# Optimization experiments

Hardware: AMD Instinct MI355X
Metric: run time of the kernel (lower is better)

Reference implementation:

```python
import jax, jax.numpy as jnp
import numpy as np

TEMPERATURE = 0.07

def _l2norm(x):
    return x / jnp.linalg.norm(x, axis=-1, keepdims=True)

def setup_inputs() -> dict:
    key = jax.random.key(0)
    k1, k2, k3, k4 = jax.random.split(key, 4)
    B, T, C_ctx, C_enc, P, K = 8, 256, 512, 256, 12, 128
    context = jax.random.normal(k1, (B, T, C_ctx), dtype=jnp.float32)
    encoded = jax.random.normal(k2, (B, T, C_enc), dtype=jnp.float32)
    W = jax.random.normal(k3, (P, C_enc, C_ctx), dtype=jnp.float32) * (1.0 / np.sqrt(C_ctx))
    neg_idx = jax.random.randint(k4, (P, B * (T - 1), K), 0, B * T, dtype=jnp.int64)
    return {"context": context, "encoded": encoded, "W": W, "neg_idx": neg_idx}

def reference(context, encoded, W, neg_idx):
    B, T, C_enc = encoded.shape
    n_pred = W.shape[0]
    # normalized pool of all encoded vectors [B*T, C_enc]
    pool = _l2norm(encoded.reshape(B * T, C_enc))
    total = jnp.float32(0.0)
    for k in range(1, n_pred + 1):  # fixed small loop over horizons
        Nk = B * (T - k)
        c_t = context[:, : T - k, :]                       # [B, T-k, C_ctx]
        z_hat = jnp.einsum('btc,ec->bte', c_t, W[k - 1])   # [B, T-k, C_enc]
        z_hat = _l2norm(z_hat.reshape(Nk, C_enc))
        z_pos = _l2norm(encoded[:, k:, :].reshape(Nk, C_enc))
        pos_logits = jnp.sum(z_hat * z_pos, axis=-1, keepdims=True)  # [Nk, 1]
        z_neg = pool[neg_idx[k - 1, :Nk]]                  # [Nk, K, C_enc]
        neg_logits = jnp.einsum('nc,nkc->nk', z_hat, z_neg)
        logits = jnp.concatenate([pos_logits, neg_logits], axis=1) / TEMPERATURE
        # cross-entropy with target class 0
        step_loss = jnp.mean(jax.nn.logsumexp(logits, axis=-1) - logits[:, 0])
        total = total + step_loss
    return total / n_pred
```

## Files before the change

kernel.cpp:

```cpp
#include <hip/hip_runtime.h>
#include <hip/hip_bf16.h>

typedef __attribute__((ext_vector_type(8))) short short8;
typedef __attribute__((ext_vector_type(4))) float f32x4;
typedef _Float16 __attribute__((ext_vector_type(2))) half2v;

#define INV_TEMP 14.285714285714286f
#define LOGIT_MAX 14.2857143f
#define L2E 1.44269504f
#define OFFE (LOGIT_MAX * L2E)
#define PCLIP 0.23f
#define PDELTA (PCLIP / 7.f)
#define PQS (7.f / PCLIP)

__device__ __forceinline__ ushort bf16c(float f) {
  uint u = __float_as_uint(f);
  uint r = (u + 0x7fffu + ((u >> 16) & 1u)) >> 16;
  return (ushort)r;
}
__device__ __forceinline__ uint pk2(float a, float b) {
  return (uint)bf16c(a) | ((uint)bf16c(b) << 16);
}
__device__ __forceinline__ uint pkh(float a, float b) {
  return __builtin_bit_cast(uint, __builtin_amdgcn_cvt_pkrtz(a, b));
}
__device__ __forceinline__ half2v h2(uint u) {
  return __builtin_bit_cast(half2v, u);
}
__device__ __forceinline__ int sdot4_(uint a, uint b, int c) {
  return __builtin_amdgcn_sdot4((int)a, (int)b, c, false);
}
__device__ __forceinline__ void gl_lds16(const void* g, void* l) {
  __builtin_amdgcn_global_load_lds(
      (const __attribute__((address_space(1))) void*)g,
      (__attribute__((address_space(3))) void*)l, 16, 0, 0);
}

template <int CTRL>
__device__ __forceinline__ float dpp_add(float v) {
  const int x = __builtin_amdgcn_mov_dpp(__float_as_int(v), CTRL, 0xF, 0xF, true);
  return v + __int_as_float(x);
}
template <int CTRL>
__device__ __forceinline__ int dpp_addi(int v) {
  return v + __builtin_amdgcn_mov_dpp(v, CTRL, 0xF, 0xF, true);
}
__device__ __forceinline__ float qsum16(float v) {
  v = dpp_add<0xB1>(v);
  v = dpp_add<0x4E>(v);
  v = dpp_add<0x141>(v);
  v = dpp_add<0x140>(v);
  return v;
}
__device__ __forceinline__ int qsum8i(int v) {
  v = dpp_addi<0xB1>(v);
  v = dpp_addi<0x4E>(v);
  v = dpp_addi<0x141>(v);
  return v;
}

__global__ __launch_bounds__(256) void prep_kernel(
    const float* __restrict__ ctx, const float* __restrict__ W,
    const float* __restrict__ enc, ushort* __restrict__ ctxb,
    ushort* __restrict__ Wb, uint* __restrict__ pool4,
    float* __restrict__ acc) {
  const int bid = blockIdx.x;
  const int tid = threadIdx.x;
  if (bid < 1280) {
    const float* in;
    ushort* out;
    size_t i;
    if (bid < 512) { in = ctx; out = ctxb; i = (size_t)bid * 256 + tid; }
    else           { in = W;   out = Wb;   i = (size_t)(bid - 512) * 256 + tid; }
    const float4 a = *(const float4*)(in + i * 8);
    const float4 b = *(const float4*)(in + i * 8 + 4);
    const uint4 o = make_uint4(pk2(a.x, a.y), pk2(a.z, a.w), pk2(b.x, b.y), pk2(b.z, b.w));
    *(uint4*)(out + i * 8) = o;
    return;
  }
  if (bid == 1280 && tid < 12) acc[tid] = 0.f;
  const int grp = tid >> 4, lane = tid & 15;
  const int r = (bid - 1280) * 16 + grp;
  const float* src = enc + (size_t)r * 256 + lane * 16;
  float4 v0 = *(const float4*)(src);
  float4 v1 = *(const float4*)(src + 4);
  float4 v2 = *(const float4*)(src + 8);
  float4 v3 = *(const float4*)(src + 12);
  float c[16] = {v0.x, v0.y, v0.z, v0.w, v1.x, v1.y, v1.z, v1.w,
                 v2.x, v2.y, v2.z, v2.w, v3.x, v3.y, v3.z, v3.w};
  float ss = 0.f;
#pragma unroll
  for (int i = 0; i < 16; ++i) ss = fmaf(c[i], c[i], ss);
  ss = qsum16(ss);
  const float qs = rsqrtf(ss) * PQS;
  uint w0 = 0, w1 = 0;
#pragma unroll
  for (int n = 0; n < 8; ++n) {
    const int q0 = (int)rintf(fminf(fmaxf(c[n] * qs, -7.f), 7.f)) + 8;
    const int q1 = (int)rintf(fminf(fmaxf(c[8 + n] * qs, -7.f), 7.f)) + 8;
    w0 |= (uint)q0 << (4 * n);
    w1 |= (uint)q1 << (4 * n);
  }
  *(uint2*)(pool4 + (size_t)r * 32 + lane * 2) = make_uint2(w0, w1);
}

__global__ __launch_bounds__(256) void zhat_gemm_kernel(
    const ushort* __restrict__ ctxb, const ushort* __restrict__ Wb,
    uint* __restrict__ Zp) {
  const int kk = blockIdx.z;
  const int Tk = 255 - kk, Nk = 8 * Tk;
  const int rowbase = blockIdx.y * 64;
  if (rowbase >= Nk) return;
  const int colbase = blockIdx.x * 128;

  __shared__ __attribute__((aligned(16))) ushort As[2][64 * 32];
  __shared__ __attribute__((aligned(16))) ushort Bs[2][128 * 32];

  const int tid = threadIdx.x;
  const int wid = tid >> 6, lane = tid & 63;
  const int arow = tid & 63;
  int n = rowbase + arow;
  if (n >= Nk) n = Nk - 1;
  const int bb = n / Tk, tt = n - bb * Tk;
  const ushort* aptr = ctxb + ((size_t)(bb * 256 + tt)) * 512 + (tid >> 6) * 8;
  const int brow = tid & 127;
  const ushort* bptr = Wb + ((size_t)kk * 256 + colbase + brow) * 512 + (tid >> 7) * 8;

  const int wm = wid >> 1, wn = wid & 1;
  const int l15 = lane & 15, l16 = lane >> 4;
  const int wboff = wid * 1024;

  f32x4 acc[2][4];
#pragma unroll
  for (int i = 0; i < 2; ++i)
#pragma unroll
    for (int j = 0; j < 4; ++j) acc[i][j] = (f32x4){0.f, 0.f, 0.f, 0.f};

  const size_t aoff = (size_t)(l16 * 64 + wm * 32 + l15) * 8;
  const size_t boff = (size_t)(l16 * 128 + wn * 64 + l15) * 8;

#define STAGE(B, K0)                                              \
  gl_lds16(aptr + (K0), (char*)As[B] + wboff);                    \
  gl_lds16(bptr + (K0), (char*)Bs[B] + wboff);                    \
  gl_lds16(bptr + (K0) + 16, (char*)Bs[B] + wboff + 4096);

#define SYNCPT                                                    \
  asm volatile("s_waitcnt vmcnt(0)" ::: "memory");                \
  __builtin_amdgcn_s_barrier();                                   \
  __builtin_amdgcn_sched_barrier(0);

#define COMPUTE(B)                                                              \
  {                                                                             \
    const ushort* ar = As[B] + aoff;                                            \
    const ushort* br = Bs[B] + boff;                                            \
    short8 bf[4];                                                               \
    bf[0] = *(const short8*)(br);                                               \
    bf[1] = *(const short8*)(br + 128);                                         \
    bf[2] = *(const short8*)(br + 256);                                         \
    bf[3] = *(const short8*)(br + 384);                                         \
    const short8 a0 = *(const short8*)(ar);                                     \
    const short8 a1 = *(const short8*)(ar + 128);                               \
    _Pragma("unroll")                                                           \
    for (int nb = 0; nb < 4; ++nb) {                                            \
      acc[0][nb] = __builtin_amdgcn_mfma_f32_16x16x32_bf16(a0, bf[nb], acc[0][nb], 0, 0, 0); \
      acc[1][nb] = __builtin_amdgcn_mfma_f32_16x16x32_bf16(a1, bf[nb], acc[1][nb], 0, 0, 0); \
    }                                                                           \
  }

  STAGE(0, 0)
  SYNCPT
  for (int k0 = 0; k0 < 512; k0 += 64) {
    STAGE(1, k0 + 32)
    COMPUTE(0)
    SYNCPT
    if (k0 + 64 < 512) { STAGE(0, k0 + 64) }
    COMPUTE(1)
    SYNCPT
  }
#undef STAGE
#undef SYNCPT
#undef COMPUTE

#pragma unroll
  for (int mb = 0; mb < 2; ++mb) {
    const int row0 = rowbase + wm * 32 + mb * 16 + l16 * 4;
#pragma unroll
    for (int r = 0; r < 4; ++r) {
      const int row = row0 + r;
      if (row < Nk) {
        uint* zp = Zp + ((size_t)kk * 2040 + row) * 128 + (colbase >> 1) + wn * 32 + l15;
        zp[0]  = pkh(acc[mb][0][r], acc[mb][1][r]);
        zp[16] = pkh(acc[mb][2][r], acc[mb][3][r]);
      }
    }
  }
}

#define DOTN(P) ({                                                              \
    int d0_ = 0, d1_ = 0;                                                       \
    uint e_, o_;                                                                \
    e_ = P.x & 0x0F0F0F0Fu; o_ = (P.x >> 4) & 0x0F0F0F0Fu;                      \
    d0_ = sdot4_(zq[0], e_, d0_); d1_ = sdot4_(zq[4], o_, d1_);                 \
    e_ = P.y & 0x0F0F0F0Fu; o_ = (P.y >> 4) & 0x0F0F0F0Fu;                      \
    d0_ = sdot4_(zq[1], e_, d0_); d1_ = sdot4_(zq[5], o_, d1_);                 \
    e_ = P.z & 0x0F0F0F0Fu; o_ = (P.z >> 4) & 0x0F0F0F0Fu;                      \
    d0_ = sdot4_(zq[2], e_, d0_); d1_ = sdot4_(zq[6], o_, d1_);                 \
    e_ = P.w & 0x0F0F0F0Fu; o_ = (P.w >> 4) & 0x0F0F0F0Fu;                      \
    d0_ = sdot4_(zq[3], e_, d0_); d1_ = sdot4_(zq[7], o_, d1_);                 \
    qsum8i(d0_ + d1_); })

#define LDB(P, IDX) P = *(const uint4*)(pbase + (size_t)(uint)(IDX) * 32);
#define ACCB(SUM, P) SUM += exp2f(fmaf((float)DOTN(P), kG, c2m));

__global__ __launch_bounds__(256) void loss_kernel(
    const uint* __restrict__ Zp, const uint* __restrict__ pool4,
    const int* __restrict__ neg_idx, float* __restrict__ acc) {
  const int kk = blockIdx.y;
  const int Tk = 255 - kk, Nk = 8 * Tk;
  if ((int)(blockIdx.x * 16) >= Nk) return;
  const int tid = threadIdx.x;
  const int n = blockIdx.x * 16 + (tid >> 4);
  const int l = tid & 15;
  const int h = l >> 3;
  const int g = l & 7;
  float row_loss = 0.f;
  if (n < Nk) {
    const uint* zr = Zp + ((size_t)kk * 2040 + n) * 128 + g * 16;
    uint zu[16];
#pragma unroll
    for (int i = 0; i < 4; ++i) *(uint4*)(zu + 4 * i) = *(const uint4*)(zr + 4 * i);
    float zf[32];
#pragma unroll
    for (int c = 0; c < 16; ++c) {
      const half2v hv = h2(zu[c]);
      zf[c] = (float)hv.x;
      zf[16 + c] = (float)hv.y;
    }
    float ss = 0.f;
#pragma unroll
    for (int i = 0; i < 32; ++i) ss = fmaf(zf[i], zf[i], ss);
    ss = dpp_add<0xB1>(ss); ss = dpp_add<0x4E>(ss); ss = dpp_add<0x141>(ss);
    const float s127 = rsqrtf(ss) * 127.f;
    uint zq[8];
#pragma unroll
    for (int t = 0; t < 4; ++t) {
      const uint e0 = (uint)((int)rintf(zf[8 * t]     * s127) & 255);
      const uint e1 = (uint)((int)rintf(zf[8 * t + 2] * s127) & 255);
      const uint e2 = (uint)((int)rintf(zf[8 * t + 4] * s127) & 255);
      const uint e3 = (uint)((int)rintf(zf[8 * t + 6] * s127) & 255);
      zq[t] = e0 | (e1 << 8) | (e2 << 16) | (e3 << 24);
      const uint o0 = (uint)((int)rintf(zf[8 * t + 1] * s127) & 255);
      const uint o1 = (uint)((int)rintf(zf[8 * t + 3] * s127) & 255);
      const uint o2 = (uint)((int)rintf(zf[8 * t + 5] * s127) & 255);
      const uint o3 = (uint)((int)rintf(zf[8 * t + 7] * s127) & 255);
      zq[t + 4] = o0 | (o1 << 8) | (o2 << 16) | (o3 << 24);
    }
    int nq = 0, zs = 0;
#pragma unroll
    for (int t = 0; t < 8; ++t) {
      nq = sdot4_(zq[t], zq[t], nq);
      zs = sdot4_(zq[t], 0x01010101u, zs);
    }
    nq = qsum8i(nq);
    zs = qsum8i(zs);
    const float kG = (INV_TEMP * L2E * PDELTA) * rsqrtf((float)nq);
    const float c2 = -8.f * (float)zs * kG;
    const float c2m = c2 - OFFE;

    const uint* pbase = pool4 + g * 4;
    const int bb = n / Tk, tt = n - bb * Tk;
    uint4 PP;
    LDB(PP, bb * 256 + tt + kk + 1)
    const float pose = fmaf((float)DOTN(PP), kG, c2);

    const int* ip = neg_idx + ((size_t)kk * 2040 + n) * 128 + h * 64;
    float s0 = 0.f, s1 = 0.f, s2 = 0.f, s3 = 0.f;
    uint4 A, B, C, D, E, F, G, H;
    {
      const int4 iv = *(const int4*)ip;
      LDB(A, iv.x) LDB(B, iv.y) LDB(C, iv.z) LDB(D, iv.w)
    }
    for (int j8 = 0; j8 < 8; ++j8) {
      {
        const int4 jv = *(const int4*)(ip + j8 * 8 + 4);
        LDB(E, jv.x) LDB(F, jv.y) LDB(G, jv.z) LDB(H, jv.w)
      }
      ACCB(s0, A) ACCB(s1, B) ACCB(s2, C) ACCB(s3, D)
      if (j8 < 7) {
        const int4 kv = *(const int4*)(ip + j8 * 8 + 8);
        LDB(A, kv.x) LDB(B, kv.y) LDB(C, kv.z) LDB(D, kv.w)
      }
      ACCB(s0, E) ACCB(s1, F) ACCB(s2, G) ACCB(s3, H)
    }
    float sl = (s0 + s1) + (s2 + s3);
    sl = dpp_add<0x140>(sl);
    const float ssum = sl + exp2f(pose - OFFE);
    row_loss = LOGIT_MAX + 0.69314718f * (__log2f(ssum) - pose);
  }
  __shared__ float bl[16];
  if (l == 0) bl[tid >> 4] = row_loss;
  __syncthreads();
  if (tid == 0) {
    float s = 0.f;
#pragma unroll
    for (int i = 0; i < 16; ++i) s += bl[i];
    atomicAdd(&acc[kk], s);
  }
}

__global__ void finalize_kernel(const float* __restrict__ acc,
                                float* __restrict__ out) {
  if (threadIdx.x == 0) {
    float tot = 0.f;
#pragma unroll
    for (int kk = 0; kk < 12; ++kk) tot += acc[kk] / (8.0f * (255 - kk));
    out[0] = tot / 12.0f;
  }
}

extern "C" void kernel_launch(void* const* d_in, const int* in_sizes, int n_in,
                              void* d_out, int out_size, void* d_ws, size_t ws_size,
                              hipStream_t stream) {
  const float* ctx = (const float*)d_in[0];
  const float* enc = (const float*)d_in[1];
  const float* W   = (const float*)d_in[2];
  const int*   neg = (const int*)d_in[3];
  float* out = (float*)d_out;

  char* ws = (char*)d_ws;
  uint*   pool4 = (uint*)(ws);
  ushort* ctxb  = (ushort*)(ws + 262144);
  ushort* Wb    = (ushort*)(ws + 2359296);
  uint*   Zp    = (uint*)(ws + 5505024);
  float*  accb  = (float*)(ws + 18038784);

  prep_kernel<<<dim3(1408), dim3(256), 0, stream>>>(ctx, W, enc, ctxb, Wb, pool4, accb);
  zhat_gemm_kernel<<<dim3(2, 32, 12), dim3(256), 0, stream>>>(ctxb, Wb, Zp);
  loss_kernel<<<dim3(128, 12), dim3(256), 0, stream>>>(Zp, pool4, neg, accb);
  finalize_kernel<<<dim3(1), dim3(64), 0, stream>>>(accb, out);
}
```

Baseline: 66.44 us.

## Use int4 sdot8 dot products in loss kernel and fuse finalize via counter

When the sdot8 builtin is available, z_hat is quantized to signed int4 instead of int8. Each negative-pool dot product then becomes four sdot8 ops on nibble-packed data, with an XOR to re-bias the pool codes. This replaces the mask/shift unpacking and eight sdot4 ops per dot. The separate finalize kernel is also removed: the last loss block, detected with an atomic counter, computes the final mean, saving one launch. The cost is coarser z_hat quantization, which may reduce loss accuracy, plus a threadfence and extra atomics per block.

```diff
diff --git a/kernel.cpp b/kernel.cpp
--- a/kernel.cpp
+++ b/kernel.cpp
@@ -13,6 +13,12 @@
 #define PDELTA (PCLIP / 7.f)
 #define PQS (7.f / PCLIP)
 
+#if __has_builtin(__builtin_amdgcn_sdot8)
+#define HAVE_SDOT8 1
+#else
+#define HAVE_SDOT8 0
+#endif
+
 __device__ __forceinline__ ushort bf16c(float f) {
   uint u = __float_as_uint(f);
   uint r = (u + 0x7fffu + ((u >> 16) & 1u)) >> 16;
@@ -30,6 +36,11 @@
 __device__ __forceinline__ int sdot4_(uint a, uint b, int c) {
   return __builtin_amdgcn_sdot4((int)a, (int)b, c, false);
 }
+#if HAVE_SDOT8
+__device__ __forceinline__ int sdot8_(uint a, uint b, int c) {
+  return __builtin_amdgcn_sdot8((int)a, (int)b, c, false);
+}
+#endif
 __device__ __forceinline__ void gl_lds16(const void* g, void* l) {
   __builtin_amdgcn_global_load_lds(
       (const __attribute__((address_space(1))) void*)g,
@@ -63,7 +74,7 @@
     const float* __restrict__ ctx, const float* __restrict__ W,
     const float* __restrict__ enc, ushort* __restrict__ ctxb,
     ushort* __restrict__ Wb, uint* __restrict__ pool4,
-    float* __restrict__ acc) {
+    float* __restrict__ acc, int* __restrict__ cnt) {
   const int bid = blockIdx.x;
   const int tid = threadIdx.x;
   if (bid < 1280) {
@@ -78,7 +89,10 @@
     *(uint4*)(out + i * 8) = o;
     return;
   }
-  if (bid == 1280 && tid < 12) acc[tid] = 0.f;
+  if (bid == 1280) {
+    if (tid < 12) acc[tid] = 0.f;
+    if (tid == 12) *cnt = 0;
+  }
   const int grp = tid >> 4, lane = tid & 15;
   const int r = (bid - 1280) * 16 + grp;
   const float* src = enc + (size_t)r * 256 + lane * 16;
@@ -196,6 +210,15 @@
   }
 }
 
+#if HAVE_SDOT8
+#define DOTN(P) ({                                                              \
+    int d_ = 0;                                                                 \
+    d_ = sdot8_(zq4[0], P.x ^ 0x88888888u, d_);                                 \
+    d_ = sdot8_(zq4[1], P.y ^ 0x88888888u, d_);                                 \
+    d_ = sdot8_(zq4[2], P.z ^ 0x88888888u, d_);                                 \
+    d_ = sdot8_(zq4[3], P.w ^ 0x88888888u, d_);                                 \
+    qsum8i(d_); })
+#else
 #define DOTN(P) ({                                                              \
     int d0_ = 0, d1_ = 0;                                                       \
     uint e_, o_;                                                                \
@@ -208,16 +231,17 @@
     e_ = P.w & 0x0F0F0F0Fu; o_ = (P.w >> 4) & 0x0F0F0F0Fu;                      \
     d0_ = sdot4_(zq[3], e_, d0_); d1_ = sdot4_(zq[7], o_, d1_);                 \
     qsum8i(d0_ + d1_); })
+#endif
 
 #define LDB(P, IDX) P = *(const uint4*)(pbase + (size_t)(uint)(IDX) * 32);
 #define ACCB(SUM, P) SUM += exp2f(fmaf((float)DOTN(P), kG, c2m));
 
 __global__ __launch_bounds__(256) void loss_kernel(
     const uint* __restrict__ Zp, const uint* __restrict__ pool4,
-    const int* __restrict__ neg_idx, float* __restrict__ acc) {
+    const int* __restrict__ neg_idx, float* __restrict__ acc,
+    int* __restrict__ cnt, float* __restrict__ out) {
   const int kk = blockIdx.y;
   const int Tk = 255 - kk, Nk = 8 * Tk;
-  if ((int)(blockIdx.x * 16) >= Nk) return;
   const int tid = threadIdx.x;
   const int n = blockIdx.x * 16 + (tid >> 4);
   const int l = tid & 15;
@@ -240,6 +264,28 @@
 #pragma unroll
     for (int i = 0; i < 32; ++i) ss = fmaf(zf[i], zf[i], ss);
     ss = dpp_add<0xB1>(ss); ss = dpp_add<0x4E>(ss); ss = dpp_add<0x141>(ss);
+
+#if HAVE_SDOT8
+    const float s_z = rsqrtf(ss) * PQS;
+    uint zq4[4];
+#pragma unroll
+    for (int j = 0; j < 4; ++j) {
+      uint w = 0;
+#pragma unroll
+      for (int n2 = 0; n2 < 8; ++n2) {
+        const int q = (int)rintf(fminf(fmaxf(zf[8 * j + n2] * s_z, -7.f), 7.f));
+        w |= ((uint)(q & 15)) << (4 * n2);
+      }
+      zq4[j] = w;
+    }
+    int nq = 0;
+#pragma unroll
+    for (int j = 0; j < 4; ++j) nq = sdot8_(zq4[j], zq4[j], nq);
+    nq = qsum8i(nq);
+    const float kG = (INV_TEMP * L2E * PDELTA) * rsqrtf((float)nq);
+    const float c2m = -OFFE;
+    const float poseb = 0.f;
+#else
     const float s127 = rsqrtf(ss) * 127.f;
     uint zq[8];
 #pragma unroll
@@ -264,14 +310,15 @@
     nq = qsum8i(nq);
     zs = qsum8i(zs);
     const float kG = (INV_TEMP * L2E * PDELTA) * rsqrtf((float)nq);
-    const float c2 = -8.f * (float)zs * kG;
-    const float c2m = c2 - OFFE;
+    const float poseb = -8.f * (float)zs * kG;
+    const float c2m = poseb - OFFE;
+#endif
 
     const uint* pbase = pool4 + g * 4;
     const int bb = n / Tk, tt = n - bb * Tk;
     uint4 PP;
     LDB(PP, bb * 256 + tt + kk + 1)
-    const float pose = fmaf((float)DOTN(PP), kG, c2);
+    const float pose = fmaf((float)DOTN(PP), kG, poseb);
 
     const int* ip = neg_idx + ((size_t)kk * 2040 + n) * 128 + h * 64;
     float s0 = 0.f, s1 = 0.f, s2 = 0.f, s3 = 0.f;
@@ -305,16 +352,15 @@
 #pragma unroll
     for (int i = 0; i < 16; ++i) s += bl[i];
     atomicAdd(&acc[kk], s);
-  }
-}
-
-__global__ void finalize_kernel(const float* __restrict__ acc,
-                                float* __restrict__ out) {
-  if (threadIdx.x == 0) {
-    float tot = 0.f;
-#pragma unroll
-    for (int kk = 0; kk < 12; ++kk) tot += acc[kk] / (8.0f * (255 - kk));
-    out[0] = tot / 12.0f;
+    __threadfence();
+    const int old = atomicAdd(cnt, 1);
+    if (old == 12 * 128 - 1) {
+      float tot = 0.f;
+#pragma unroll
+      for (int k2 = 0; k2 < 12; ++k2)
+        tot += atomicAdd(&acc[k2], 0.0f) / (8.0f * (255 - k2));
+      out[0] = tot / 12.0f;
+    }
   }
 }
 
@@ -333,9 +379,9 @@
   ushort* Wb    = (ushort*)(ws + 2359296);
   uint*   Zp    = (uint*)(ws + 5505024);
   float*  accb  = (float*)(ws + 18038784);
-
-  prep_kernel<<<dim3(1408), dim3(256), 0, stream>>>(ctx, W, enc, ctxb, Wb, pool4, accb);
+  int*    cnt   = (int*)(ws + 18038832);
+
+  prep_kernel<<<dim3(1408), dim3(256), 0, stream>>>(ctx, W, enc, ctxb, Wb, pool4, accb, cnt);
   zhat_gemm_kernel<<<dim3(2, 32, 12), dim3(256), 0, stream>>>(ctxb, Wb, Zp);
-  loss_kernel<<<dim3(128, 12), dim3(256), 0, stream>>>(Zp, pool4, neg, accb);
-  finalize_kernel<<<dim3(1), dim3(64), 0, stream>>>(accb, out);
-}
+  loss_kernel<<<dim3(128, 12), dim3(256), 0, stream>>>(Zp, pool4, neg, accb, cnt, out);
+}
```

After: 93.64 us. 41.0% more time.
